# Kernel optimization log

Measured on AMD Instinct MI355X. Metric: run time of the kernel, lower is better.

The kernel has to match this reference:

```python
import jax, jax.numpy as jnp
import numpy as np

B, S, D, H, L, FF = 1, 2048, 512, 8, 4, 2048
DH = D // H


def _sincos(n, d):
    theta = 1.0 / (10000.0 ** (np.arange(0, d, 2, dtype=np.float64) / d))
    ang = np.arange(n, dtype=np.float64)[:, None] * theta[None, :]
    sin = np.repeat(np.sin(ang), 2, axis=-1).astype(np.float32)
    cos = np.repeat(np.cos(ang), 2, axis=-1).astype(np.float32)
    return jnp.asarray(sin), jnp.asarray(cos)  # [n, d]


def _rot(x):
    # rotate pairs: (x1, x2) -> (-x2, x1), interleaved
    x1, x2 = x[..., 0::2], x[..., 1::2]
    return jnp.stack([-x2, x1], axis=-1).reshape(x.shape)


def _theta_shift(x, sin, cos):
    return x * cos + _rot(x) * sin


def _decay_mask(n, h):
    # RetNet per-head decay gammas: 1 - exp(linspace(log(1/32), log(1/512), h))
    gammas = 1.0 - np.exp(np.linspace(np.log(1.0 / 32.0), np.log(1.0 / 512.0), h))
    dist = np.arange(n)[:, None] - np.arange(n)[None, :]
    m = np.where(dist >= 0, gammas[:, None, None] ** np.maximum(dist, 0), 0.0)
    return jnp.asarray(m, dtype=jnp.float32)  # [h, n, n]


def _ln(x, w, b, eps=1e-5):
    mu = x.mean(-1, keepdims=True)
    var = ((x - mu) ** 2).mean(-1, keepdims=True)
    return (x - mu) * jax.lax.rsqrt(var + eps) * w + b


def setup_inputs() -> dict:
    key = jax.random.key(0)
    ks = jax.random.split(key, 12)
    sc = 0.02
    nrm = lambda k, shp: jax.random.normal(k, shp, jnp.float32) * sc
    return {
        "x": jax.random.normal(ks[0], (B, S, D), jnp.float32),
        "pos_emb": nrm(ks[1], (5000, D)),
        "Wq": nrm(ks[2], (L, D, D)), "bq": jnp.zeros((L, D), jnp.float32),
        "Wk": nrm(ks[3], (L, D, D)), "bk": jnp.zeros((L, D), jnp.float32),
        "Wv": nrm(ks[4], (L, D, D)), "bv": jnp.zeros((L, D), jnp.float32),
        "Wg": nrm(ks[5], (L, D, D)), "bg": jnp.zeros((L, D), jnp.float32),
        "Wo": nrm(ks[6], (L, D, D)), "bo": jnp.zeros((L, D), jnp.float32),
        "ln1w": jnp.ones((L, D), jnp.float32), "ln1b": jnp.zeros((L, D), jnp.float32),
        "ln2w": jnp.ones((L, D), jnp.float32), "ln2b": jnp.zeros((L, D), jnp.float32),
        "W1": nrm(ks[7], (L, D, FF)), "b1": jnp.zeros((L, FF), jnp.float32),
        "W2": nrm(ks[8], (L, FF, D)), "b2": jnp.zeros((L, D), jnp.float32),
        "Wout": nrm(ks[9], (D, 1)), "bout": jnp.zeros((1,), jnp.float32),
    }


def reference(x, pos_emb, Wq, bq, Wk, bk, Wv, bv, Wg, bg, Wo, bo,
              ln1w, ln1b, ln2w, ln2b, W1, b1, W2, b2, Wout, bout):
    b, s, d = x.shape
    # faithful to source: pos_emb[:x.shape[0]] (requires B==1 to broadcast)
    x = x + pos_emb[: x.shape[0]]
    sin, cos = _sincos(s, DH)
    dmask = _decay_mask(s, H)  # [h, s, s]
    inv_scale = 1.0 / jnp.sqrt(jnp.float32(DH))

    def heads(t):  # [b,s,d] -> [b,h,s,dh]
        return t.reshape(b, s, H, DH).transpose(0, 2, 1, 3)

    for l in range(L):
        # --- multi-scale retention block (pre-LN) ---
        y = _ln(x, ln1w[l], ln1b[l])
        q = heads(y @ Wq[l] + bq[l])
        k = heads(y @ Wk[l] + bk[l])
        v = heads(y @ Wv[l] + bv[l])
        q = _theta_shift(q, sin, cos) * inv_scale
        k = _theta_shift(k, sin, cos)
        sim = jnp.einsum("bhnd,bhmd->bhnm", q, k) * dmask  # decay-masked QK^T
        ret = jnp.einsum("bhnm,bhmd->bhnd", sim, v)
        # per-head group norm (no affine)
        mu = ret.mean(-1, keepdims=True)
        var = ((ret - mu) ** 2).mean(-1, keepdims=True)
        ret = (ret - mu) * jax.lax.rsqrt(var + 1e-6)
        ret = ret.transpose(0, 2, 1, 3).reshape(b, s, d)
        g = jax.nn.silu(y @ Wg[l] + bg[l])
        x = x + (g * ret) @ Wo[l] + bo[l]
        # --- FFN block (pre-LN, swish) ---
        z = _ln(x, ln2w[l], ln2b[l])
        x = x + jax.nn.silu(z @ W1[l] + b1[l]) @ W2[l] + b2[l]

    return jax.nn.sigmoid(x @ Wout + bout)  # [b, s, 1]
```

## Files before the change

### kernel.cpp

```cpp
#include <hip/hip_runtime.h>
#include <math.h>
#include <stdint.h>

#define SEQ 2048
#define DMODEL 512
#define NH 8
#define DHEAD 64
#define NL 4
#define DFF 2048

typedef __attribute__((ext_vector_type(8))) short short8;
typedef __attribute__((ext_vector_type(4))) float f32x4;

__device__ __forceinline__ short f2bf(float f) {
  unsigned u = __float_as_uint(f);
  u += 0x7fffu + ((u >> 16) & 1u);
  return (short)(u >> 16);
}
__device__ __forceinline__ float silu_f(float x) { return x / (1.f + __expf(-x)); }

__device__ __forceinline__ void cp16(const void* g, void* l) {
  __builtin_amdgcn_global_load_lds(
      (const __attribute__((address_space(1))) unsigned*)(unsigned long long)(uintptr_t)g,
      (__attribute__((address_space(3))) unsigned*)(unsigned)(uintptr_t)l, 16, 0, 0);
}

struct TP { const float* src; short* dst; int rows, cols, base, lstride; };
struct TPs { TP t[7]; };
__global__ __launch_bounds__(256) void k_prep(TPs ts) {
  int bid = blockIdx.x;
  int di = 6;
  while (di > 0 && bid < ts.t[di].base) --di;
  TP d = ts.t[di];
  int local = bid - d.base;
  int tx = d.cols >> 5, ty = d.rows >> 5;
  int tpz = tx * ty;
  int z = local / tpz, rem = local - z * tpz;
  int bx = (rem % tx) * 32, by = (rem / tx) * 32;
  const float* src = d.src + (size_t)z * d.rows * d.cols;
  short* dst = d.dst + (size_t)z * d.lstride;
  __shared__ float tile[32][33];
  int txi = threadIdx.x & 31, tyi = threadIdx.x >> 5;
#pragma unroll
  for (int k = 0; k < 4; ++k)
    tile[tyi + k * 8][txi] = src[(size_t)(by + tyi + k * 8) * d.cols + bx + txi];
  __syncthreads();
#pragma unroll
  for (int k = 0; k < 4; ++k)
    dst[(size_t)(bx + tyi + k * 8) * d.rows + by + txi] = f2bf(tile[txi][tyi + k * 8]);
}

__global__ void k_init(const float* __restrict__ xi, const float* __restrict__ pos, float* __restrict__ xo,
                       float* __restrict__ sn, float* __restrict__ cs) {
  if (blockIdx.x < 1024) {
    int i = blockIdx.x * 256 + threadIdx.x;
    float4 a = ((const float4*)xi)[i];
    float4 p = ((const float4*)pos)[i & 127];
    a.x += p.x; a.y += p.y; a.z += p.z; a.w += p.w;
    ((float4*)xo)[i] = a;
  } else {
    int g = (blockIdx.x - 1024) * 256 + threadIdx.x;
    int s = g >> 5, p = g & 31;
    double inv = pow(10000.0, -(double)p / 32.0);
    double a = (double)s * inv;
    float sv = (float)sin(a), cv = (float)cos(a);
    sn[s * DHEAD + 2 * p] = sv; sn[s * DHEAD + 2 * p + 1] = sv;
    cs[s * DHEAD + 2 * p] = cv; cs[s * DHEAD + 2 * p + 1] = cv;
  }
}

__global__ __launch_bounds__(256) void k_ln(const float* __restrict__ x, const float* __restrict__ parts, int np,
                                            const float* __restrict__ w, const float* __restrict__ b,
                                            short* __restrict__ o, float eps, float* __restrict__ xout) {
  int wid = threadIdx.x >> 6, lane = threadIdx.x & 63;
  int row = blockIdx.x * 4 + wid;
  size_t base = (size_t)row * DMODEL + lane * 8;
  float4 v0 = *(const float4*)(x + base);
  float4 v1 = *(const float4*)(x + base + 4);
  for (int p = 0; p < np; ++p) {
    const float* pp = parts + (size_t)p * SEQ * DMODEL;
    float4 a0 = *(const float4*)(pp + base);
    float4 a1 = *(const float4*)(pp + base + 4);
    v0.x += a0.x; v0.y += a0.y; v0.z += a0.z; v0.w += a0.w;
    v1.x += a1.x; v1.y += a1.y; v1.z += a1.z; v1.w += a1.w;
  }
  if (xout) {
    *(float4*)(xout + base) = v0;
    *(float4*)(xout + base + 4) = v1;
  }
  float sm = v0.x + v0.y + v0.z + v0.w + v1.x + v1.y + v1.z + v1.w;
  float sq = v0.x * v0.x + v0.y * v0.y + v0.z * v0.z + v0.w * v0.w +
             v1.x * v1.x + v1.y * v1.y + v1.z * v1.z + v1.w * v1.w;
#pragma unroll
  for (int m = 1; m < 64; m <<= 1) { sm += __shfl_xor(sm, m); sq += __shfl_xor(sq, m); }
  float mu = sm * (1.f / 512.f);
  float rstd = rsqrtf(sq * (1.f / 512.f) - mu * mu + eps);
  const float* wr = w + lane * 8; const float* br = b + lane * 8;
  float vals[8] = {v0.x, v0.y, v0.z, v0.w, v1.x, v1.y, v1.z, v1.w};
  short t[8] __attribute__((aligned(16)));
#pragma unroll
  for (int i = 0; i < 8; ++i) t[i] = f2bf((vals[i] - mu) * rstd * wr[i] + br[i]);
  *(int4*)(o + (size_t)row * DMODEL + lane * 8) = *(int4*)t;
}

struct GB { const short* Bt; const float* bias; void* out; int mode; };
struct GP {
  const short* A;
  const float* sn; const float* cs;
  GB b[4];
  int M, N, K, kspl, wide;
};

template <int BN>
__global__ __launch_bounds__(256) void k_gemm(GP ga) {
  constexpr int NBW = BN / 32;
  constexpr int ARND = 4;
  constexpr int BRND = BN / 32;
  const int z = blockIdx.z;
  GB gb; int k0, klen;
  if (ga.kspl > 0) { gb = ga.b[0]; k0 = z * ga.kspl; klen = ga.kspl; }
  else { gb = ga.b[0]; k0 = 0; klen = ga.K; }
  const int K = ga.K, N = ga.N, M = ga.M;
  const int n0 = blockIdx.x * BN, m0 = blockIdx.y * 128;
  if (ga.wide) gb = ga.b[n0 >> 9];
  const int tid = threadIdx.x;
  const int w = tid >> 6, lane = tid & 63, l16 = lane & 15, quad = lane >> 4;
  const int wm = (w & 1) * 64, wn = (w >> 1) * (BN / 2);
  const int nIter = klen >> 6;

  __shared__ __align__(16) short As[2][8192];
  __shared__ __align__(16) short Bs[2][BN * 64];

  const short* Ab = ga.A + (size_t)m0 * K + k0;
  const short* Bb = gb.Bt + (size_t)n0 * K + k0;
  const int rsub = lane >> 3, cch = (lane & 7) ^ rsub;

  auto stage = [&](int buf, int it) {
#pragma unroll
    for (int c = 0; c < ARND; ++c) {
      int seg = w + 4 * c;
      cp16(Ab + (size_t)(seg * 8 + rsub) * K + (it << 6) + cch * 8, &As[buf][seg * 512]);
    }
#pragma unroll
    for (int c = 0; c < BRND; ++c) {
      int seg = w + 4 * c;
      cp16(Bb + (size_t)(seg * 8 + rsub) * K + (it << 6) + cch * 8, &Bs[buf][seg * 512]);
    }
  };

  f32x4 acc[4][NBW];
#pragma unroll
  for (int a = 0; a < 4; ++a)
#pragma unroll
    for (int b = 0; b < NBW; ++b) acc[a][b] = {0.f, 0.f, 0.f, 0.f};

  stage(0, 0);
  for (int it = 0; it < nIter; ++it) {
    __syncthreads();
    if (it + 1 < nIter) stage((it + 1) & 1, it + 1);
    const short* as = As[it & 1];
    const short* bs = Bs[it & 1];
#pragma unroll
    for (int kki = 0; kki < 2; ++kki) {
      int ch = ((quad + 4 * kki) ^ (l16 & 7)) * 8;
      short8 af[4], bfv[NBW];
#pragma unroll
      for (int a = 0; a < 4; ++a) af[a] = *(const short8*)&as[(wm + a * 16 + l16) * 64 + ch];
#pragma unroll
      for (int b = 0; b < NBW; ++b) bfv[b] = *(const short8*)&bs[(wn + b * 16 + l16) * 64 + ch];
#pragma unroll
      for (int a = 0; a < 4; ++a)
#pragma unroll
        for (int b = 0; b < NBW; ++b)
          acc[a][b] = __builtin_amdgcn_mfma_f32_16x16x32_bf16(af[a], bfv[b], acc[a][b], 0, 0, 0);
    }
  }

  const int mode = gb.mode;
#pragma unroll
  for (int a = 0; a < 4; ++a) {
#pragma unroll
    for (int b = 0; b < NBW; ++b) {
      int row0 = m0 + wm + a * 16 + quad * 4;
      int col = n0 + wn + b * 16 + l16;
      int colO = ga.wide ? (col & 511) : col;
      float bi = (mode == 2 && z > 0) ? 0.f : gb.bias[colO];
      float vals[4];
#pragma unroll
      for (int r = 0; r < 4; ++r) vals[r] = acc[a][b][r] + bi;
      if (mode == 5 || mode == 6) {
        float sc = (mode == 5) ? 0.125f : 1.f;
        int d = colO & 63;
#pragma unroll
        for (int r = 0; r < 4; ++r) {
          int s = row0 + r;
          float vv = vals[r];
          float p = __shfl_xor(vv, 1);
          float rot = (colO & 1) ? p : -p;
          float o = (vv * ga.cs[s * 64 + d] + rot * ga.sn[s * 64 + d]) * sc;
          ((short*)gb.out)[(size_t)s * DMODEL + colO] = f2bf(o);
        }
      } else if (mode == 4) {
        short t4[4] __attribute__((aligned(8)));
#pragma unroll
        for (int r = 0; r < 4; ++r) t4[r] = f2bf(vals[r]);
        *(uint2*)&((short*)gb.out)[(size_t)colO * M + row0] = *(const uint2*)t4;
      } else if (mode == 0) {
#pragma unroll
        for (int r = 0; r < 4; ++r) ((float*)gb.out)[(size_t)(row0 + r) * DMODEL + colO] = vals[r];
      } else if (mode == 1) {
#pragma unroll
        for (int r = 0; r < 4; ++r) ((short*)gb.out)[(size_t)(row0 + r) * N + col] = f2bf(silu_f(vals[r]));
      } else {
        float* po = (float*)gb.out + (size_t)z * M * DMODEL;
#pragma unroll
        for (int r = 0; r < 4; ++r) po[(size_t)(row0 + r) * DMODEL + colO] = vals[r];
      }
    }
  }
}

__global__ __launch_bounds__(256) void k_attn(const short* __restrict__ qb, const short* __restrict__ kb,
                                              const short* __restrict__ vtb, float* __restrict__ r0,
                                              float* __restrict__ r1) {
  int x = blockIdx.x, hd = blockIdx.y, jc = blockIdx.z;
  int ib = jc ? (31 - x) : x;
  int t = threadIdx.x;
  int w = t >> 6, lane = t & 63, l16 = lane & 15, quad = lane >> 4;
  __shared__ __align__(16) short smem[4 * 64 * 72];
  short* qs = smem;
  short* kt = smem + 4608;
  short* vt = smem + 9216;
  short* p  = smem + 13824;

  double stepd = (log(1.0 / 512.0) - log(1.0 / 32.0)) / 7.0;
  double gam = 1.0 - exp(log(1.0 / 32.0) + hd * stepd);
  float l2g = (float)(log(gam) * 1.4426950408889634);

  for (int c = t; c < 512; c += 256) {
    int r = c >> 3, d8 = (c & 7) * 8;
    *(short8*)&qs[r * 72 + d8] = *(const short8*)&qb[(size_t)(ib * 64 + r) * DMODEL + hd * DHEAD + d8];
  }
  f32x4 oacc[4];
#pragma unroll
  for (int b = 0; b < 4; ++b) oacc[b] = {0.f, 0.f, 0.f, 0.f};

  for (int jb = jc; jb <= ib; jb += 2) {
    __syncthreads();
    for (int c = t; c < 512; c += 256) {
      int r = c >> 3, d8 = (c & 7) * 8;
      *(short8*)&kt[r * 72 + d8] = *(const short8*)&kb[(size_t)(jb * 64 + r) * DMODEL + hd * DHEAD + d8];
      *(short8*)&vt[r * 72 + d8] = *(const short8*)&vtb[(size_t)(hd * DHEAD + r) * SEQ + jb * 64 + d8];
    }
    __syncthreads();
    f32x4 sacc[4];
#pragma unroll
    for (int b = 0; b < 4; ++b) sacc[b] = {0.f, 0.f, 0.f, 0.f};
#pragma unroll
    for (int kk = 0; kk < 64; kk += 32) {
      short8 af = *(const short8*)&qs[(w * 16 + l16) * 72 + kk + quad * 8];
#pragma unroll
      for (int b = 0; b < 4; ++b) {
        short8 bf_ = *(const short8*)&kt[(b * 16 + l16) * 72 + kk + quad * 8];
        sacc[b] = __builtin_amdgcn_mfma_f32_16x16x32_bf16(af, bf_, sacc[b], 0, 0, 0);
      }
    }
    int dtile = (ib - jb) * 64;
#pragma unroll
    for (int b = 0; b < 4; ++b) {
#pragma unroll
      for (int r = 0; r < 4; ++r) {
        int iloc = w * 16 + quad * 4 + r;
        int jloc = b * 16 + l16;
        int df = dtile + iloc - jloc;
        float dec = (df < 0) ? 0.f : exp2f(l2g * (float)df);
        p[iloc * 72 + jloc] = f2bf(sacc[b][r] * dec);
      }
    }
    __syncthreads();
#pragma unroll
    for (int kk = 0; kk < 64; kk += 32) {
      short8 af = *(const short8*)&vt[(w * 16 + l16) * 72 + kk + quad * 8];
#pragma unroll
      for (int b = 0; b < 4; ++b) {
        short8 bf_ = *(const short8*)&p[(b * 16 + l16) * 72 + kk + quad * 8];
        oacc[b] = __builtin_amdgcn_mfma_f32_16x16x32_bf16(af, bf_, oacc[b], 0, 0, 0);
      }
    }
  }
  __syncthreads();
  float* obuf = (float*)smem;
#pragma unroll
  for (int b = 0; b < 4; ++b) {
#pragma unroll
    for (int r = 0; r < 4; ++r) {
      int d = w * 16 + quad * 4 + r;
      int i = b * 16 + l16;
      obuf[i * 68 + d] = oacc[b][r];
    }
  }
  __syncthreads();
  float* rp = jc ? r1 : r0;
  for (int c = t; c < 1024; c += 256) {
    int r = c >> 4, d4 = (c & 15) * 4;
    *(float4*)&rp[(size_t)(ib * 64 + r) * DMODEL + hd * DHEAD + d4] = *(const float4*)&obuf[r * 68 + d4];
  }
}

__global__ __launch_bounds__(256) void k_retgate(const float* __restrict__ r0, const float* __restrict__ r1,
                                                 const float* __restrict__ g, short* __restrict__ o) {
  int wid = threadIdx.x >> 6, lane = threadIdx.x & 63;
  int row = blockIdx.x * 4 + wid;
  int s = row >> 3, hd = row & 7;
  size_t base = (size_t)s * DMODEL + hd * DHEAD + lane;
  float v = r0[base] + r1[base];
  float sm = v, sq = v * v;
#pragma unroll
  for (int m = 1; m < 64; m <<= 1) { sm += __shfl_xor(sm, m); sq += __shfl_xor(sq, m); }
  float mu = sm * (1.f / 64.f);
  float var = sq * (1.f / 64.f) - mu * mu;
  float rn = (v - mu) * rsqrtf(var + 1e-6f);
  o[base] = f2bf(silu_f(g[base]) * rn);
}

__global__ __launch_bounds__(256) void k_final(const float* __restrict__ x, const float* __restrict__ parts, int np,
                                               const float* __restrict__ w, const float* __restrict__ bo,
                                               float* __restrict__ o) {
  int wid = threadIdx.x >> 6, lane = threadIdx.x & 63;
  int row = blockIdx.x * 4 + wid;
  size_t base = (size_t)row * DMODEL + lane * 8;
  float4 a0 = *(const float4*)(x + base), a1 = *(const float4*)(x + base + 4);
  for (int p = 0; p < np; ++p) {
    const float* pp = parts + (size_t)p * SEQ * DMODEL;
    float4 b0 = *(const float4*)(pp + base);
    float4 b1 = *(const float4*)(pp + base + 4);
    a0.x += b0.x; a0.y += b0.y; a0.z += b0.z; a0.w += b0.w;
    a1.x += b1.x; a1.y += b1.y; a1.z += b1.z; a1.w += b1.w;
  }
  float4 w0 = *(const float4*)(w + lane * 8), w1 = *(const float4*)(w + lane * 8 + 4);
  float sm = a0.x * w0.x + a0.y * w0.y + a0.z * w0.z + a0.w * w0.w +
             a1.x * w1.x + a1.y * w1.y + a1.z * w1.z + a1.w * w1.w;
#pragma unroll
  for (int m = 1; m < 64; m <<= 1) sm += __shfl_xor(sm, m);
  if (lane == 0) o[row] = 1.f / (1.f + __expf(-(sm + bo[0])));
}

extern "C" void kernel_launch(void* const* d_in, const int* in_sizes, int n_in,
                              void* d_out, int out_size, void* d_ws, size_t ws_size,
                              hipStream_t stream) {
  const float* x_in = (const float*)d_in[0];
  const float* pos = (const float*)d_in[1];
  const float* Wq = (const float*)d_in[2];  const float* bq = (const float*)d_in[3];
  const float* Wk = (const float*)d_in[4];  const float* bk = (const float*)d_in[5];
  const float* Wv = (const float*)d_in[6];  const float* bv = (const float*)d_in[7];
  const float* Wg = (const float*)d_in[8];  const float* bg = (const float*)d_in[9];
  const float* Wo = (const float*)d_in[10]; const float* bo = (const float*)d_in[11];
  const float* ln1w = (const float*)d_in[12]; const float* ln1b = (const float*)d_in[13];
  const float* ln2w = (const float*)d_in[14]; const float* ln2b = (const float*)d_in[15];
  const float* W1 = (const float*)d_in[16]; const float* b1 = (const float*)d_in[17];
  const float* W2 = (const float*)d_in[18]; const float* b2 = (const float*)d_in[19];
  const float* Wout = (const float*)d_in[20]; const float* bout = (const float*)d_in[21];
  float* out = (float*)d_out;

  char* ws = (char*)d_ws;
  size_t off = 0;
  auto alloc = [&](size_t bytes) -> void* {
    void* p = ws + off;
    off += (bytes + 255) & ~(size_t)255;
    return p;
  };
  const size_t DD = (size_t)DMODEL * DMODEL;
  const size_t SD = (size_t)SEQ * DMODEL;
  short* wqkvg = (short*)alloc((size_t)NL * 4 * DD * 2);
  short* wot = (short*)alloc((size_t)NL * DD * 2);
  short* w1t = (short*)alloc((size_t)NL * DMODEL * DFF * 2);
  short* w2t = (short*)alloc((size_t)NL * DMODEL * DFF * 2);
  float* xb = (float*)alloc(SD * 4);
  short* ybf = (short*)alloc(SD * 2);
  float* graw = (float*)alloc(SD * 4);
  short* qb = (short*)alloc(SD * 2);
  short* kb = (short*)alloc(SD * 2);
  short* vtb = (short*)alloc(SD * 2);
  float* ret0 = (float*)alloc(SD * 4);
  float* ret1 = (float*)alloc(SD * 4);
  short* grb = (short*)alloc(SD * 2);
  short* zbf = (short*)alloc(SD * 2);
  short* hbf = (short*)alloc((size_t)SEQ * DFF * 2);
  float* sint = (float*)alloc((size_t)SEQ * DHEAD * 4);
  float* cost = (float*)alloc((size_t)SEQ * DHEAD * 4);
  float* wpart = (float*)alloc(2 * SD * 4);
  float* fpart = (float*)alloc(4 * SD * 4);

  TPs tp;
  tp.t[0] = TP{Wq, wqkvg + 0 * DD, DMODEL, DMODEL, 0, (int)(4 * DD)};
  tp.t[1] = TP{Wk, wqkvg + 1 * DD, DMODEL, DMODEL, 1024, (int)(4 * DD)};
  tp.t[2] = TP{Wv, wqkvg + 2 * DD, DMODEL, DMODEL, 2048, (int)(4 * DD)};
  tp.t[3] = TP{Wg, wqkvg + 3 * DD, DMODEL, DMODEL, 3072, (int)(4 * DD)};
  tp.t[4] = TP{Wo, wot, DMODEL, DMODEL, 4096, (int)DD};
  tp.t[5] = TP{W1, w1t, DMODEL, DFF, 5120, DMODEL * DFF};
  tp.t[6] = TP{W2, w2t, DFF, DMODEL, 9216, DMODEL * DFF};
  k_prep<<<13312, 256, 0, stream>>>(tp);
  k_init<<<1280, 256, 0, stream>>>(x_in, pos, xb, sint, cost);

  for (int l = 0; l < NL; ++l) {
    k_ln<<<SEQ / 4, 256, 0, stream>>>(xb, fpart, l == 0 ? 0 : 4,
                                      ln1w + l * DMODEL, ln1b + l * DMODEL, ybf, 1e-5f,
                                      l == 0 ? nullptr : xb);

    GP gq{};
    gq.A = ybf; gq.sn = sint; gq.cs = cost;
    gq.b[0] = GB{wqkvg + (size_t)l * 4 * DD, bq + l * DMODEL, qb, 5};
    gq.b[1] = GB{wqkvg + (size_t)l * 4 * DD, bk + l * DMODEL, kb, 6};
    gq.b[2] = GB{wqkvg + (size_t)l * 4 * DD, bv + l * DMODEL, vtb, 4};
    gq.b[3] = GB{wqkvg + (size_t)l * 4 * DD, bg + l * DMODEL, graw, 0};
    gq.M = SEQ; gq.N = 4 * DMODEL; gq.K = DMODEL; gq.kspl = 0; gq.wide = 1;
    k_gemm<128><<<dim3(16, SEQ / 128, 1), 256, 0, stream>>>(gq);

    k_attn<<<dim3(32, NH, 2), 256, 0, stream>>>(qb, kb, vtb, ret0, ret1);
    k_retgate<<<SEQ * NH / 4, 256, 0, stream>>>(ret0, ret1, graw, grb);

    GP gw{};
    gw.A = grb;
    gw.b[0] = GB{wot + l * DD, bo + l * DMODEL, wpart, 2};
    gw.M = SEQ; gw.N = DMODEL; gw.K = DMODEL; gw.kspl = 256; gw.wide = 0;
    k_gemm<64><<<dim3(DMODEL / 64, SEQ / 128, 2), 256, 0, stream>>>(gw);

    k_ln<<<SEQ / 4, 256, 0, stream>>>(xb, wpart, 2,
                                      ln2w + l * DMODEL, ln2b + l * DMODEL, zbf, 1e-5f, xb);

    GP g1{};
    g1.A = zbf;
    g1.b[0] = GB{w1t + (size_t)l * DMODEL * DFF, b1 + l * DFF, hbf, 1};
    g1.M = SEQ; g1.N = DFF; g1.K = DMODEL; g1.kspl = 0; g1.wide = 0;
    k_gemm<128><<<dim3(DFF / 128, SEQ / 128, 1), 256, 0, stream>>>(g1);

    GP g2{};
    g2.A = hbf;
    g2.b[0] = GB{w2t + (size_t)l * DMODEL * DFF, b2 + l * DMODEL, fpart, 2};
    g2.M = SEQ; g2.N = DMODEL; g2.K = DFF; g2.kspl = 512; g2.wide = 0;
    k_gemm<64><<<dim3(DMODEL / 64, SEQ / 128, 4), 256, 0, stream>>>(g2);
  }
  k_final<<<SEQ / 4, 256, 0, stream>>>(xb, fpart, 4, Wout, bout, out);
}
```

Measured before the change: 570.5 us.

## Fuse retention gating into attention, fold init into prep/LN, halve GEMM M-tile

Removes k_init by moving the sin/cos table build and the counter reset into k_prep, and by adding the positional embedding inside the first layer-norm. The separate retgate kernel is removed: each attention half-block bumps an atomic counter, and the second block to finish combines both partial results, then applies group norm and the SiLU gate. GEMM tiles shrink from 128 to 64 rows, doubling the grid to fill more CUs. The trade-offs are extra atomics and fences in the attention kernel and lower per-block data reuse in the GEMMs.

Result: slower. 946.5 us (+65.9%).

```diff
diff --git a/kernel.cpp b/kernel.cpp
--- a/kernel.cpp
+++ b/kernel.cpp
@@ -27,8 +27,23 @@
 
 struct TP { const float* src; short* dst; int rows, cols, base, lstride; };
 struct TPs { TP t[7]; };
-__global__ __launch_bounds__(256) void k_prep(TPs ts) {
+__global__ __launch_bounds__(256) void k_prep(TPs ts, float* __restrict__ sn, float* __restrict__ cs,
+                                              int* __restrict__ cnt) {
   int bid = blockIdx.x;
+  if (bid >= 13312) {
+    int g = (bid - 13312) * 256 + threadIdx.x;
+    if (bid == 13312) {
+#pragma unroll
+      for (int j = 0; j < 4; ++j) cnt[threadIdx.x * 4 + j] = 0;
+    }
+    int s = g >> 5, p = g & 31;
+    double inv = pow(10000.0, -(double)p / 32.0);
+    double a = (double)s * inv;
+    float sv = (float)sin(a), cv = (float)cos(a);
+    sn[s * DHEAD + 2 * p] = sv; sn[s * DHEAD + 2 * p + 1] = sv;
+    cs[s * DHEAD + 2 * p] = cv; cs[s * DHEAD + 2 * p + 1] = cv;
+    return;
+  }
   int di = 6;
   while (di > 0 && bid < ts.t[di].base) --di;
   TP d = ts.t[di];
@@ -50,33 +65,21 @@
     dst[(size_t)(bx + tyi + k * 8) * d.rows + by + txi] = f2bf(tile[txi][tyi + k * 8]);
 }
 
-__global__ void k_init(const float* __restrict__ xi, const float* __restrict__ pos, float* __restrict__ xo,
-                       float* __restrict__ sn, float* __restrict__ cs) {
-  if (blockIdx.x < 1024) {
-    int i = blockIdx.x * 256 + threadIdx.x;
-    float4 a = ((const float4*)xi)[i];
-    float4 p = ((const float4*)pos)[i & 127];
-    a.x += p.x; a.y += p.y; a.z += p.z; a.w += p.w;
-    ((float4*)xo)[i] = a;
-  } else {
-    int g = (blockIdx.x - 1024) * 256 + threadIdx.x;
-    int s = g >> 5, p = g & 31;
-    double inv = pow(10000.0, -(double)p / 32.0);
-    double a = (double)s * inv;
-    float sv = (float)sin(a), cv = (float)cos(a);
-    sn[s * DHEAD + 2 * p] = sv; sn[s * DHEAD + 2 * p + 1] = sv;
-    cs[s * DHEAD + 2 * p] = cv; cs[s * DHEAD + 2 * p + 1] = cv;
-  }
-}
-
 __global__ __launch_bounds__(256) void k_ln(const float* __restrict__ x, const float* __restrict__ parts, int np,
                                             const float* __restrict__ w, const float* __restrict__ b,
-                                            short* __restrict__ o, float eps, float* __restrict__ xout) {
+                                            short* __restrict__ o, float eps, float* __restrict__ xout,
+                                            const float* __restrict__ pos) {
   int wid = threadIdx.x >> 6, lane = threadIdx.x & 63;
   int row = blockIdx.x * 4 + wid;
   size_t base = (size_t)row * DMODEL + lane * 8;
   float4 v0 = *(const float4*)(x + base);
   float4 v1 = *(const float4*)(x + base + 4);
+  if (pos) {
+    float4 p0 = *(const float4*)(pos + lane * 8);
+    float4 p1 = *(const float4*)(pos + lane * 8 + 4);
+    v0.x += p0.x; v0.y += p0.y; v0.z += p0.z; v0.w += p0.w;
+    v1.x += p1.x; v1.y += p1.y; v1.z += p1.z; v1.w += p1.w;
+  }
   for (int p = 0; p < np; ++p) {
     const float* pp = parts + (size_t)p * SEQ * DMODEL;
     float4 a0 = *(const float4*)(pp + base);
@@ -114,21 +117,19 @@
 template <int BN>
 __global__ __launch_bounds__(256) void k_gemm(GP ga) {
   constexpr int NBW = BN / 32;
-  constexpr int ARND = 4;
   constexpr int BRND = BN / 32;
   const int z = blockIdx.z;
+  const int n0 = blockIdx.x * BN, m0 = blockIdx.y * 64;
   GB gb; int k0, klen;
   if (ga.kspl > 0) { gb = ga.b[0]; k0 = z * ga.kspl; klen = ga.kspl; }
-  else { gb = ga.b[0]; k0 = 0; klen = ga.K; }
+  else { gb = ga.wide ? ga.b[n0 >> 9] : ga.b[z]; k0 = 0; klen = ga.K; }
   const int K = ga.K, N = ga.N, M = ga.M;
-  const int n0 = blockIdx.x * BN, m0 = blockIdx.y * 128;
-  if (ga.wide) gb = ga.b[n0 >> 9];
   const int tid = threadIdx.x;
   const int w = tid >> 6, lane = tid & 63, l16 = lane & 15, quad = lane >> 4;
-  const int wm = (w & 1) * 64, wn = (w >> 1) * (BN / 2);
+  const int wm = (w & 1) * 32, wn = (w >> 1) * (BN / 2);
   const int nIter = klen >> 6;
 
-  __shared__ __align__(16) short As[2][8192];
+  __shared__ __align__(16) short As[2][4096];
   __shared__ __align__(16) short Bs[2][BN * 64];
 
   const short* Ab = ga.A + (size_t)m0 * K + k0;
@@ -137,7 +138,7 @@
 
   auto stage = [&](int buf, int it) {
 #pragma unroll
-    for (int c = 0; c < ARND; ++c) {
+    for (int c = 0; c < 2; ++c) {
       int seg = w + 4 * c;
       cp16(Ab + (size_t)(seg * 8 + rsub) * K + (it << 6) + cch * 8, &As[buf][seg * 512]);
     }
@@ -148,9 +149,9 @@
     }
   };
 
-  f32x4 acc[4][NBW];
-#pragma unroll
-  for (int a = 0; a < 4; ++a)
+  f32x4 acc[2][NBW];
+#pragma unroll
+  for (int a = 0; a < 2; ++a)
 #pragma unroll
     for (int b = 0; b < NBW; ++b) acc[a][b] = {0.f, 0.f, 0.f, 0.f};
 
@@ -163,13 +164,13 @@
 #pragma unroll
     for (int kki = 0; kki < 2; ++kki) {
       int ch = ((quad + 4 * kki) ^ (l16 & 7)) * 8;
-      short8 af[4], bfv[NBW];
-#pragma unroll
-      for (int a = 0; a < 4; ++a) af[a] = *(const short8*)&as[(wm + a * 16 + l16) * 64 + ch];
+      short8 af[2], bfv[NBW];
+#pragma unroll
+      for (int a = 0; a < 2; ++a) af[a] = *(const short8*)&as[(wm + a * 16 + l16) * 64 + ch];
 #pragma unroll
       for (int b = 0; b < NBW; ++b) bfv[b] = *(const short8*)&bs[(wn + b * 16 + l16) * 64 + ch];
 #pragma unroll
-      for (int a = 0; a < 4; ++a)
+      for (int a = 0; a < 2; ++a)
 #pragma unroll
         for (int b = 0; b < NBW; ++b)
           acc[a][b] = __builtin_amdgcn_mfma_f32_16x16x32_bf16(af[a], bfv[b], acc[a][b], 0, 0, 0);
@@ -178,7 +179,7 @@
 
   const int mode = gb.mode;
 #pragma unroll
-  for (int a = 0; a < 4; ++a) {
+  for (int a = 0; a < 2; ++a) {
 #pragma unroll
     for (int b = 0; b < NBW; ++b) {
       int row0 = m0 + wm + a * 16 + quad * 4;
@@ -222,12 +223,14 @@
 
 __global__ __launch_bounds__(256) void k_attn(const short* __restrict__ qb, const short* __restrict__ kb,
                                               const short* __restrict__ vtb, float* __restrict__ r0,
-                                              float* __restrict__ r1) {
+                                              float* __restrict__ r1, const float* __restrict__ graw,
+                                              short* __restrict__ grb, int* __restrict__ cnt) {
   int x = blockIdx.x, hd = blockIdx.y, jc = blockIdx.z;
   int ib = jc ? (31 - x) : x;
   int t = threadIdx.x;
   int w = t >> 6, lane = t & 63, l16 = lane & 15, quad = lane >> 4;
   __shared__ __align__(16) short smem[4 * 64 * 72];
+  __shared__ int second;
   short* qs = smem;
   short* kt = smem + 4608;
   short* vt = smem + 9216;
@@ -305,22 +308,25 @@
     int r = c >> 4, d4 = (c & 15) * 4;
     *(float4*)&rp[(size_t)(ib * 64 + r) * DMODEL + hd * DHEAD + d4] = *(const float4*)&obuf[r * 68 + d4];
   }
-}
-
-__global__ __launch_bounds__(256) void k_retgate(const float* __restrict__ r0, const float* __restrict__ r1,
-                                                 const float* __restrict__ g, short* __restrict__ o) {
-  int wid = threadIdx.x >> 6, lane = threadIdx.x & 63;
-  int row = blockIdx.x * 4 + wid;
-  int s = row >> 3, hd = row & 7;
-  size_t base = (size_t)s * DMODEL + hd * DHEAD + lane;
-  float v = r0[base] + r1[base];
-  float sm = v, sq = v * v;
-#pragma unroll
-  for (int m = 1; m < 64; m <<= 1) { sm += __shfl_xor(sm, m); sq += __shfl_xor(sq, m); }
-  float mu = sm * (1.f / 64.f);
-  float var = sq * (1.f / 64.f) - mu * mu;
-  float rn = (v - mu) * rsqrtf(var + 1e-6f);
-  o[base] = f2bf(silu_f(g[base]) * rn);
+  __threadfence();
+  if (t == 0) second = atomicAdd(&cnt[ib * 8 + hd], 1);
+  __syncthreads();
+  if (second == 1) {
+    __threadfence();
+    const float* other = jc ? r0 : r1;
+    for (int k = 0; k < 16; ++k) {
+      int r = w * 16 + k;
+      size_t gbase = (size_t)(ib * 64 + r) * DMODEL + hd * DHEAD + lane;
+      float v = obuf[r * 68 + lane] + other[gbase];
+      float sm = v, sq = v * v;
+#pragma unroll
+      for (int m = 1; m < 64; m <<= 1) { sm += __shfl_xor(sm, m); sq += __shfl_xor(sq, m); }
+      float mu = sm * (1.f / 64.f);
+      float var = sq * (1.f / 64.f) - mu * mu;
+      float rn = (v - mu) * rsqrtf(var + 1e-6f);
+      grb[gbase] = f2bf(silu_f(graw[gbase]) * rn);
+    }
+  }
 }
 
 __global__ __launch_bounds__(256) void k_final(const float* __restrict__ x, const float* __restrict__ parts, int np,
@@ -390,6 +396,7 @@
   float* cost = (float*)alloc((size_t)SEQ * DHEAD * 4);
   float* wpart = (float*)alloc(2 * SD * 4);
   float* fpart = (float*)alloc(4 * SD * 4);
+  int* cnt = (int*)alloc(NL * 256 * 4);
 
   TPs tp;
   tp.t[0] = TP{Wq, wqkvg + 0 * DD, DMODEL, DMODEL, 0, (int)(4 * DD)};
@@ -399,13 +406,12 @@
   tp.t[4] = TP{Wo, wot, DMODEL, DMODEL, 4096, (int)DD};
   tp.t[5] = TP{W1, w1t, DMODEL, DFF, 5120, DMODEL * DFF};
   tp.t[6] = TP{W2, w2t, DFF, DMODEL, 9216, DMODEL * DFF};
-  k_prep<<<13312, 256, 0, stream>>>(tp);
-  k_init<<<1280, 256, 0, stream>>>(x_in, pos, xb, sint, cost);
+  k_prep<<<13568, 256, 0, stream>>>(tp, sint, cost, cnt);
 
   for (int l = 0; l < NL; ++l) {
-    k_ln<<<SEQ / 4, 256, 0, stream>>>(xb, fpart, l == 0 ? 0 : 4,
+    k_ln<<<SEQ / 4, 256, 0, stream>>>(l == 0 ? x_in : xb, fpart, l == 0 ? 0 : 4,
                                       ln1w + l * DMODEL, ln1b + l * DMODEL, ybf, 1e-5f,
-                                      l == 0 ? nullptr : xb);
+                                      xb, l == 0 ? pos : nullptr);
 
     GP gq{};
     gq.A = ybf; gq.sn = sint; gq.cs = cost;
@@ -414,31 +420,30 @@
     gq.b[2] = GB{wqkvg + (size_t)l * 4 * DD, bv + l * DMODEL, vtb, 4};
     gq.b[3] = GB{wqkvg + (size_t)l * 4 * DD, bg + l * DMODEL, graw, 0};
     gq.M = SEQ; gq.N = 4 * DMODEL; gq.K = DMODEL; gq.kspl = 0; gq.wide = 1;
-    k_gemm<128><<<dim3(16, SEQ / 128, 1), 256, 0, stream>>>(gq);
-
-    k_attn<<<dim3(32, NH, 2), 256, 0, stream>>>(qb, kb, vtb, ret0, ret1);
-    k_retgate<<<SEQ * NH / 4, 256, 0, stream>>>(ret0, ret1, graw, grb);
+    k_gemm<128><<<dim3(16, SEQ / 64, 1), 256, 0, stream>>>(gq);
+
+    k_attn<<<dim3(32, NH, 2), 256, 0, stream>>>(qb, kb, vtb, ret0, ret1, graw, grb, cnt + l * 256);
 
     GP gw{};
     gw.A = grb;
     gw.b[0] = GB{wot + l * DD, bo + l * DMODEL, wpart, 2};
     gw.M = SEQ; gw.N = DMODEL; gw.K = DMODEL; gw.kspl = 256; gw.wide = 0;
-    k_gemm<64><<<dim3(DMODEL / 64, SEQ / 128, 2), 256, 0, stream>>>(gw);
+    k_gemm<64><<<dim3(DMODEL / 64, SEQ / 64, 2), 256, 0, stream>>>(gw);
 
     k_ln<<<SEQ / 4, 256, 0, stream>>>(xb, wpart, 2,
-                                      ln2w + l * DMODEL, ln2b + l * DMODEL, zbf, 1e-5f, xb);
+                                      ln2w + l * DMODEL, ln2b + l * DMODEL, zbf, 1e-5f, xb, nullptr);
 
     GP g1{};
     g1.A = zbf;
     g1.b[0] = GB{w1t + (size_t)l * DMODEL * DFF, b1 + l * DFF, hbf, 1};
     g1.M = SEQ; g1.N = DFF; g1.K = DMODEL; g1.kspl = 0; g1.wide = 0;
-    k_gemm<128><<<dim3(DFF / 128, SEQ / 128, 1), 256, 0, stream>>>(g1);
+    k_gemm<128><<<dim3(DFF / 128, SEQ / 64, 1), 256, 0, stream>>>(g1);
 
     GP g2{};
     g2.A = hbf;
     g2.b[0] = GB{w2t + (size_t)l * DMODEL * DFF, b2 + l * DMODEL, fpart, 2};
     g2.M = SEQ; g2.N = DMODEL; g2.K = DFF; g2.kspl = 512; g2.wide = 0;
-    k_gemm<64><<<dim3(DMODEL / 64, SEQ / 128, 4), 256, 0, stream>>>(g2);
+    k_gemm<64><<<dim3(DMODEL / 64, SEQ / 64, 4), 256, 0, stream>>>(g2);
   }
   k_final<<<SEQ / 4, 256, 0, stream>>>(xb, fpart, 4, Wout, bout, out);
 }
```
